# Performance work log

Hardware: AMD Instinct MI355X
Metric: run time of the kernel (lower is better)

Reference implementation:

```python
import jax, jax.numpy as jnp
import numpy as np
import math

HEAD_NUM = 16


def _split_qkv(qkv, head_num):
    # torch: rearrange(qkv, 'b t (d k h) -> k b h t d', k=3, h=head_num)
    B, T, E3 = qkv.shape
    d = E3 // (3 * head_num)
    qkv = qkv.reshape(B, T, d, 3, head_num)        # (b,t,d,k,h)
    qkv = jnp.transpose(qkv, (3, 0, 4, 1, 2))       # (k,b,h,t,d)
    return qkv[0], qkv[1], qkv[2]


def setup_inputs() -> dict:
    key = jax.random.key(0)
    ks = jax.random.split(key, 6)
    B, T, E = 4, 1024, 1024
    return {
        "x": jax.random.normal(ks[0], (B, T, E), dtype=jnp.float32),
        "y": jax.random.normal(ks[1], (B, T, E), dtype=jnp.float32),
        "Wqkv1": jax.random.normal(ks[2], (3 * E, E), dtype=jnp.float32) * 0.02,
        "Wqkv2": jax.random.normal(ks[3], (3 * E, E), dtype=jnp.float32) * 0.02,
        "Wout1": jax.random.normal(ks[4], (E, E), dtype=jnp.float32) * 0.02,
        "Wout2": jax.random.normal(ks[5], (E, E), dtype=jnp.float32) * 0.02,
    }


def reference(x, y, Wqkv1, Wqkv2, Wout1, Wout2):
    B, T, E = x.shape
    H = HEAD_NUM
    dk = math.sqrt(E / H)

    qkv1 = x @ Wqkv1.T                              # (B,T,3E)
    qkv2 = y @ Wqkv2.T
    q1, k1, v1 = _split_qkv(qkv1, H)                # each (B,H,T,d)
    q2, k2, v2 = _split_qkv(qkv2, H)

    # cross attention: stream-2 queries attend to stream-1 keys/values and vice versa
    energy1 = jnp.einsum('bhid,bhjd->bhij', q2, k1) / dk
    energy2 = jnp.einsum('bhid,bhjd->bhij', q1, k2) / dk
    attn1 = jax.nn.softmax(energy1, axis=-1)
    attn2 = jax.nn.softmax(energy2, axis=-1)

    xo = jnp.einsum('bhij,bhjd->bhid', attn1, v1)   # (B,H,T,d)
    yo = jnp.einsum('bhij,bhjd->bhid', attn2, v2)
    xo = jnp.transpose(xo, (0, 2, 1, 3)).reshape(B, T, E)  # b t (h d)
    yo = jnp.transpose(yo, (0, 2, 1, 3)).reshape(B, T, E)

    return xo @ Wout1.T, yo @ Wout2.T
```

## Files before the change

kernel.cpp:

```cpp
#include <hip/hip_runtime.h>
#include <hip/hip_bf16.h>

typedef __hip_bfloat16 bf16;
typedef __attribute__((ext_vector_type(8))) short short8;
typedef __attribute__((ext_vector_type(4))) short short4v;
typedef __attribute__((ext_vector_type(4))) float f32x4;

#define MFMA_BF16(a, b, c) __builtin_amdgcn_mfma_f32_16x16x32_bf16((a), (b), (c), 0, 0, 0)

#define QSCALE 0.1803368860111270f

__device__ __forceinline__ short f2bf(float f) {
    union { bf16 h; short s; } u;
    u.h = __float2bfloat16(f);
    return u.s;
}

#if defined(__has_builtin) && __has_builtin(__builtin_amdgcn_cvt_pk_bf16_f32)
typedef __attribute__((ext_vector_type(2))) __bf16 bf16x2_t;
__device__ __forceinline__ unsigned int pk2(float a, float b) {
    union { bf16x2_t v; unsigned int u; } x;
    x.v = __builtin_amdgcn_cvt_pk_bf16_f32(a, b);
    return x.u;
}
#else
__device__ __forceinline__ unsigned int pk2(float a, float b) {
    union { bf16 h[2]; unsigned int u; } x;
    x.h[0] = __float2bfloat16(a);
    x.h[1] = __float2bfloat16(b);
    return x.u;
}
#endif

#if defined(__has_builtin) && __has_builtin(__builtin_amdgcn_exp2f)
#define EXP2F(x) __builtin_amdgcn_exp2f(x)
#else
#define EXP2F(x) exp2f(x)
#endif

__device__ __forceinline__ void gload16(const void* g, void* l) {
    __builtin_amdgcn_global_load_lds(
        (const __attribute__((address_space(1))) unsigned int*)g,
        (__attribute__((address_space(3))) unsigned int*)l, 16, 0, 0);
}

__global__ void cvt_fused(const float* __restrict__ x, const float* __restrict__ y,
                          const float* __restrict__ wo1, const float* __restrict__ wo2,
                          const float* __restrict__ wq1, const float* __restrict__ wq2,
                          bf16* __restrict__ ox, bf16* __restrict__ oy,
                          bf16* __restrict__ oo1, bf16* __restrict__ oo2,
                          bf16* __restrict__ oq1, bf16* __restrict__ oq2) {
    const int yb = blockIdx.y;
    if (yb < 4) {
        int i = blockIdx.x * 256 + threadIdx.x;
        const float* src; bf16* dst; int n4;
        switch (yb) {
            case 0:  src = x;   dst = ox;  n4 = 1048576; break;
            case 1:  src = y;   dst = oy;  n4 = 1048576; break;
            case 2:  src = wo1; dst = oo1; n4 = 262144;  break;
            default: src = wo2; dst = oo2; n4 = 262144;  break;
        }
        if (i >= n4) return;
        float4 f = reinterpret_cast<const float4*>(src)[i];
        short4v s;
        s.x = f2bf(f.x); s.y = f2bf(f.y); s.z = f2bf(f.z); s.w = f2bf(f.w);
        reinterpret_cast<short4v*>(dst)[i] = s;
    } else {
        const int np = blockIdx.x;
        if (np >= 3072) return;
        const int comp = np >> 10, rem = np & 1023, h = rem >> 6, d = rem & 63;
        const int srow = d * 48 + comp * 16 + h;
        const float* src = ((yb == 5) ? wq2 : wq1) + (long)srow * 1024;
        bf16* dst = ((yb == 5) ? oq2 : oq1) + (long)np * 1024;
        const float sc = (comp == 0) ? QSCALE : 1.0f;
        int t = threadIdx.x;
        float4 f = reinterpret_cast<const float4*>(src)[t];
        short4v s;
        s.x = f2bf(f.x * sc); s.y = f2bf(f.y * sc); s.z = f2bf(f.z * sc); s.w = f2bf(f.w * sc);
        reinterpret_cast<short4v*>(dst)[t] = s;
    }
}

#define GATE4 do { asm volatile("s_waitcnt vmcnt(4)" ::: "memory"); \
    __builtin_amdgcn_s_barrier(); __builtin_amdgcn_sched_barrier(0); } while (0)

__global__ __launch_bounds__(512, 2)
void gemm_qkv256(const bf16* __restrict__ A0g, const bf16* __restrict__ B0g,
                 void* o0a, void* o0b, void* o0c,
                 const bf16* __restrict__ A1g, const bf16* __restrict__ B1g,
                 void* o1a, void* o1b, void* o1c) {
    extern __shared__ short smem[];
    const int z = blockIdx.z;
    const short* A = reinterpret_cast<const short*>(z ? A1g : A0g);
    const short* B = reinterpret_cast<const short*>(z ? B1g : B0g);
    const int tid  = threadIdx.x;
    const int lane = tid & 63;
    const int w    = tid >> 6;
    const int quad = lane >> 4;
    const int l16  = lane & 15;
    const long M0 = (long)blockIdx.y * 256;
    const long N0 = (long)blockIdx.x * 256;

    const int rowblk = (w >> 2) * 64;
    const int colblk = (w & 3) * 32;
    const int cA0  = (quad ^ (l16 & 7)) * 8;
    const int aoff = (rowblk + l16) * 64;
    const int boff = 16384 + (colblk + l16) * 64;
    const int w512 = w * 512;

    const short* Asrc = A + (M0 + w * 8 + (lane >> 3)) * 1024 + ((lane & 7) ^ (lane >> 3)) * 8;
    const short* Bsrc = B + (N0 + w * 8 + (lane >> 3)) * 1024 + ((lane & 7) ^ (lane >> 3)) * 8;

    f32x4 acc[4][4][2] = {};
    short8 af[4][2], bfv[2][2];

#define SA256(half, tt, nbase) do { \
    const short* _s = Asrc + (half) * 131072 + (tt) * 64; \
    short* _d = smem + (nbase) + (half) * 8192 + w512; \
    gload16(_s, _d); gload16(_s + 65536, _d + 4096); } while (0)
#define SB256(half, tt, nbase) do { \
    const short* _s = Bsrc + (half) * 131072 + (tt) * 64; \
    short* _d = smem + (nbase) + 16384 + (half) * 8192 + w512; \
    gload16(_s, _d); gload16(_s + 65536, _d + 4096); } while (0)
#define RDA256(Ah, bbv) do { \
    _Pragma("unroll") for (int mt = 0; mt < 4; ++mt) { \
        const short* _p = &smem[(bbv) + (Ah) * 8192 + aoff + mt * 1024]; \
        af[mt][0] = *reinterpret_cast<const short8*>(_p + cA0); \
        af[mt][1] = *reinterpret_cast<const short8*>(_p + (cA0 ^ 32)); } } while (0)
#define RDB256(Bh, bbv) do { \
    _Pragma("unroll") for (int nt = 0; nt < 2; ++nt) { \
        const short* _p = &smem[(bbv) + (Bh) * 8192 + boff + nt * 1024]; \
        bfv[nt][0] = *reinterpret_cast<const short8*>(_p + cA0); \
        bfv[nt][1] = *reinterpret_cast<const short8*>(_p + (cA0 ^ 32)); } } while (0)
#define MM256(p) do { \
    __builtin_amdgcn_s_setprio(1); \
    _Pragma("unroll") for (int mt = 0; mt < 4; ++mt) \
    _Pragma("unroll") for (int nt = 0; nt < 2; ++nt) { \
        acc[p][mt][nt] = MFMA_BF16(af[mt][0], bfv[nt][0], acc[p][mt][nt]); \
        acc[p][mt][nt] = MFMA_BF16(af[mt][1], bfv[nt][1], acc[p][mt][nt]); } \
    __builtin_amdgcn_s_setprio(0); } while (0)

    SA256(0, 0, 0); SB256(0, 0, 0); SB256(1, 0, 0); SA256(1, 0, 0);

#pragma unroll 1
    for (int t = 0; t < 15; ++t) {
        const int bb = (t & 1) << 15;
        const int nb = bb ^ 32768;
        GATE4;
        SA256(0, t + 1, nb);
        RDA256(0, bb); RDB256(0, bb);
        __builtin_amdgcn_sched_barrier(0);
        MM256(0);
        GATE4;
        SB256(0, t + 1, nb);
        RDB256(1, bb);
        __builtin_amdgcn_sched_barrier(0);
        MM256(1);
        GATE4;
        SB256(1, t + 1, nb);
        RDA256(1, bb); RDB256(0, bb);
        __builtin_amdgcn_sched_barrier(0);
        MM256(2);
        SA256(1, t + 1, nb);
        RDB256(1, bb);
        __builtin_amdgcn_sched_barrier(0);
        MM256(3);
    }
    asm volatile("s_waitcnt vmcnt(0)" ::: "memory");
    __builtin_amdgcn_s_barrier();
    __builtin_amdgcn_sched_barrier(0);
    {
        const int bb = 32768;
        RDA256(0, bb); RDB256(0, bb); MM256(0);
        RDB256(1, bb); MM256(1);
        RDA256(1, bb); RDB256(0, bb); MM256(2);
        RDB256(1, bb); MM256(3);
    }

    if (blockIdx.x < 8) {
        short* dst = reinterpret_cast<short*>(blockIdx.x < 4 ? (z ? o1a : o0a)
                                                             : (z ? o1b : o0b));
        const int b = (int)(M0 >> 10);
        const int t00 = ((int)M0 & 1023);
        const int hd00 = ((int)blockIdx.x & 3) * 256;
#pragma unroll
        for (int p = 0; p < 4; ++p) {
            const int Ah = p >> 1, Bh = p & 1;
            const int tr0 = t00 + Ah * 128 + rowblk + quad * 4;
#pragma unroll
            for (int nt = 0; nt < 2; ++nt) {
                const int hd = hd00 + Bh * 128 + colblk + nt * 16 + l16;
                const int h = hd >> 6, d = hd & 63;
                short* dp = dst + (long)(b * 16 + h) * 65536 + d;
#pragma unroll
                for (int mt = 0; mt < 4; ++mt)
#pragma unroll
                    for (int r = 0; r < 4; ++r)
                        dp[(long)(tr0 + mt * 16 + r) * 64] = f2bf(acc[p][mt][nt][r]);
            }
        }
    } else {
        short* vT = reinterpret_cast<short*>(z ? o1c : o0c);
        const int b = (int)(M0 >> 10);
        const int hd00 = ((int)blockIdx.x - 8) * 256;
        short* ws = smem + w * 2304;
        const int c8 = (lane & 7) * 8;
        const int colr = lane >> 3;
#pragma unroll
        for (int p = 0; p < 4; ++p) {
            const int Ah = p >> 1, Bh = p & 1;
#pragma unroll
            for (int nt = 0; nt < 2; ++nt)
#pragma unroll
                for (int mt = 0; mt < 4; ++mt) {
                    uint2 uu;
                    uu.x = pk2(acc[p][mt][nt][0], acc[p][mt][nt][1]);
                    uu.y = pk2(acc[p][mt][nt][2], acc[p][mt][nt][3]);
                    *reinterpret_cast<uint2*>(&ws[(nt * 16 + l16) * 72 + mt * 16 + quad * 4]) = uu;
                }
            const int tb = ((int)M0 & 1023) + Ah * 128 + rowblk + c8;
#pragma unroll
            for (int q4 = 0; q4 < 4; ++q4) {
                const int col = q4 * 8 + colr;
                const int hd = hd00 + Bh * 128 + colblk + col;
                const int h = hd >> 6, d = hd & 63;
                short8 v = *reinterpret_cast<const short8*>(&ws[col * 72 + c8]);
                *reinterpret_cast<short8*>(&vT[(long)(b * 16 + h) * 65536 + (long)d * 1024 + tb]) = v;
            }
        }
    }
#undef SA256
#undef SB256
#undef RDA256
#undef RDB256
#undef MM256
}

__global__ __launch_bounds__(256)
void gemm_out(const bf16* __restrict__ A0g, const bf16* __restrict__ B0g, float* __restrict__ C0,
              const bf16* __restrict__ A1g, const bf16* __restrict__ B1g, float* __restrict__ C1) {
    __shared__ short smem2[24576];
    const int z = blockIdx.z;
    const short* A = reinterpret_cast<const short*>(z ? A1g : A0g);
    const short* B = reinterpret_cast<const short*>(z ? B1g : B0g);
    const int tid  = threadIdx.x;
    const int lane = tid & 63;
    const int w    = tid >> 6;
    const int wr   = w >> 1;
    const int wc   = w & 1;
    const int quad = lane >> 4;
    const int l16  = lane & 15;
    const long bM = (long)blockIdx.y * 128;

    f32x4 acc[4][4] = {};

    const int sr  = lane >> 2;
    const int scs = ((lane & 3) ^ (sr & 3)) * 8;
    const short* Ag0 = A + (bM + 32 * w + sr) * 1024 + scs;
    const short* Ag1 = Ag0 + 16 * 1024;
    const short* Bg0 = B + ((long)blockIdx.x * 128 + 32 * w + sr) * 1024 + scs;
    const short* Bg1 = Bg0 + 16 * 1024;
    const int sq = (quad ^ (l16 & 3)) * 8;

    {
        short* sb = smem2;
        gload16(Ag0, sb + w * 1024);
        gload16(Ag1, sb + w * 1024 + 512);
        gload16(Bg0, sb + 4096 + w * 1024);
        gload16(Bg1, sb + 4096 + w * 1024 + 512);
    }

    int bcur = 0;
#pragma unroll 1
    for (int iter = 0; iter < 32; ++iter) {
        int bnext = bcur + 1; if (bnext == 3) bnext = 0;
        if (iter < 31) {
            const int koff = (iter + 1) * 32;
            short* sb = smem2 + bnext * 8192;
            gload16(Ag0 + koff, sb + w * 1024);
            gload16(Ag1 + koff, sb + w * 1024 + 512);
            gload16(Bg0 + koff, sb + 4096 + w * 1024);
            gload16(Bg1 + koff, sb + 4096 + w * 1024 + 512);
            asm volatile("s_waitcnt vmcnt(4)" ::: "memory");
        } else {
            asm volatile("s_waitcnt vmcnt(0)" ::: "memory");
        }
        __builtin_amdgcn_s_barrier();
        __builtin_amdgcn_sched_barrier(0);

        const short* Ab = smem2 + bcur * 8192;
        const short* Bb = Ab + 4096;

        short8 af[4], bfr[4];
#pragma unroll
        for (int mt = 0; mt < 4; ++mt)
            af[mt] = *reinterpret_cast<const short8*>(&Ab[(wr * 64 + mt * 16 + l16) * 32 + sq]);
#pragma unroll
        for (int nt = 0; nt < 4; ++nt)
            bfr[nt] = *reinterpret_cast<const short8*>(&Bb[(wc * 64 + nt * 16 + l16) * 32 + sq]);
        __builtin_amdgcn_s_setprio(1);
#pragma unroll
        for (int mt = 0; mt < 4; ++mt)
#pragma unroll
            for (int nt = 0; nt < 4; ++nt)
                acc[mt][nt] = MFMA_BF16(af[mt], bfr[nt], acc[mt][nt]);
        __builtin_amdgcn_s_setprio(0);
        bcur = bnext;
    }

    float* C = z ? C1 : C0;
    const long crow = bM + wr * 64 + quad * 4;
    const long ccol = (long)blockIdx.x * 128 + wc * 64 + l16;
#pragma unroll
    for (int mt = 0; mt < 4; ++mt)
#pragma unroll
        for (int nt = 0; nt < 4; ++nt)
#pragma unroll
            for (int r = 0; r < 4; ++r)
                C[(crow + mt * 16 + r) * 1024L + ccol + nt * 16] = acc[mt][nt][r];
}

__global__ __launch_bounds__(256)
void attn_kernel(const bf16* __restrict__ q0g, const bf16* __restrict__ k0g,
                 const bf16* __restrict__ v0g, bf16* __restrict__ o0g,
                 const bf16* __restrict__ q1g, const bf16* __restrict__ k1g,
                 const bf16* __restrict__ v1g, bf16* __restrict__ o1g) {
    __shared__ short smem[24576];
    const int bh = blockIdx.x;
    const int qt = blockIdx.y;
    const int z = blockIdx.z;
    const int b = bh >> 4, h = bh & 15;
    const int tid = threadIdx.x, lane = tid & 63, w = tid >> 6;
    const int quad = lane >> 4, l16 = lane & 15;

    const short* Qb = reinterpret_cast<const short*>(z ? q1g : q0g) + (long)bh * 1024 * 64;
    const short* Kb = reinterpret_cast<const short*>(z ? k1g : k0g) + (long)bh * 1024 * 64;
    const short* Vb = reinterpret_cast<const short*>(z ? v1g : v0g) + (long)bh * 64 * 1024;
    short* Ob = reinterpret_cast<short*>(z ? o1g : o0g);

    short8 qb[2][2];
#pragma unroll
    for (int qg = 0; qg < 2; ++qg) {
        const short* Qp = Qb + (long)(qt * 128 + qg * 64 + w * 16 + l16) * 64;
        qb[qg][0] = *reinterpret_cast<const short8*>(Qp + quad * 8);
        qb[qg][1] = *reinterpret_cast<const short8*>(Qp + 32 + quad * 8);
    }

    const int r8  = lane >> 3;
    const int sc0 = ((lane & 7) ^ (r8 & 3)) * 8;
    const short* Kg0 = Kb + (long)(16 * w + r8) * 64 + sc0;
    const short* Kg1 = Kb + (long)(16 * w + 8 + r8) * 64 + (sc0 ^ 32);
    const short* Vg0 = Vb + (long)(16 * w + r8) * 1024 + sc0;
    const short* Vg1 = Vb + (long)(16 * w + 8 + r8) * 1024 + (sc0 ^ 32);

    const int jbase = 8 * (l16 >> 2) + (l16 & 3);
    const int fKs = (l16 & 3) | (((l16 >> 2) & 1) << 2);
    const int s0  = (quad ^ fKs) * 8;
    const int fVs = (l16 & 3) | (((l16 >> 3) & 1) << 2);
    const int sv  = (quad ^ fVs) * 8;

    f32x4 o[2][4] = {};
    float li[2] = {0.f, 0.f};

    gload16(Kg0, smem + w * 1024); gload16(Kg1, smem + w * 1024 + 512);
    gload16(Vg0, smem + 4096 + w * 1024); gload16(Vg1, smem + 4096 + w * 1024 + 512);

    int bcur = 0;
#pragma unroll 1
    for (int iter = 0; iter < 16; ++iter) {
        int bnext = bcur + 1; if (bnext == 3) bnext = 0;
        if (iter < 15) {
            short* sb = smem + bnext * 8192;
            const long ko = (long)(iter + 1) * 4096;
            const long vo = (long)(iter + 1) * 64;
            gload16(Kg0 + ko, sb + w * 1024);
            gload16(Kg1 + ko, sb + w * 1024 + 512);
            gload16(Vg0 + vo, sb + 4096 + w * 1024);
            gload16(Vg1 + vo, sb + 4096 + w * 1024 + 512);
            asm volatile("s_waitcnt vmcnt(4)" ::: "memory");
        } else {
            asm volatile("s_waitcnt vmcnt(0)" ::: "memory");
        }
        __builtin_amdgcn_s_barrier();
        __builtin_amdgcn_sched_barrier(0);

        const short* Ks = smem + bcur * 8192;
        const short* Vs = Ks + 4096;

        f32x4 st[2][4];
        __builtin_amdgcn_s_setprio(1);
#pragma unroll
        for (int g = 0; g < 4; ++g) {
            const int goff = (g >> 1) * 32 + (g & 1) * 4;
            const short* kr = Ks + (jbase + goff) * 64;
            short8 k0 = *reinterpret_cast<const short8*>(kr + s0);
            short8 k1 = *reinterpret_cast<const short8*>(kr + (s0 ^ 32));
#pragma unroll
            for (int qg = 0; qg < 2; ++qg) {
                f32x4 zf = {0.f, 0.f, 0.f, 0.f};
                zf = MFMA_BF16(k0, qb[qg][0], zf);
                zf = MFMA_BF16(k1, qb[qg][1], zf);
                st[qg][g] = zf;
            }
        }
        __builtin_amdgcn_s_setprio(0);

        union { unsigned int u[4]; short8 s; } f0[2], f1[2];
#pragma unroll
        for (int qg = 0; qg < 2; ++qg) {
            float p[4][4];
            float rs = 0.f;
#pragma unroll
            for (int g = 0; g < 4; ++g)
#pragma unroll
                for (int r = 0; r < 4; ++r) {
                    float e = EXP2F(st[qg][g][r]);
                    p[g][r] = e;
                    rs += e;
                }
            li[qg] += rs;
            f0[qg].u[0] = pk2(p[0][0], p[0][1]); f0[qg].u[1] = pk2(p[0][2], p[0][3]);
            f0[qg].u[2] = pk2(p[1][0], p[1][1]); f0[qg].u[3] = pk2(p[1][2], p[1][3]);
            f1[qg].u[0] = pk2(p[2][0], p[2][1]); f1[qg].u[1] = pk2(p[2][2], p[2][3]);
            f1[qg].u[2] = pk2(p[3][0], p[3][1]); f1[qg].u[3] = pk2(p[3][2], p[3][3]);
        }

        __builtin_amdgcn_s_setprio(1);
#pragma unroll
        for (int dt = 0; dt < 4; ++dt) {
            const short* vr = Vs + (dt * 16 + l16) * 64;
            short8 v0 = *reinterpret_cast<const short8*>(vr + sv);
            short8 v1 = *reinterpret_cast<const short8*>(vr + (sv ^ 32));
#pragma unroll
            for (int qg = 0; qg < 2; ++qg) {
                o[qg][dt] = MFMA_BF16(v0, f0[qg].s, o[qg][dt]);
                o[qg][dt] = MFMA_BF16(v1, f1[qg].s, o[qg][dt]);
            }
        }
        __builtin_amdgcn_s_setprio(0);
        bcur = bnext;
    }

    __syncthreads();

#pragma unroll
    for (int qg = 0; qg < 2; ++qg) {
        li[qg] += __shfl_xor(li[qg], 16);
        li[qg] += __shfl_xor(li[qg], 32);
    }

#pragma unroll
    for (int qg = 0; qg < 2; ++qg) {
        short* Os = smem + qg * 5120 + w * 1280;
        const float rl = 1.0f / li[qg];
#pragma unroll
        for (int dt = 0; dt < 4; ++dt) {
            uint2 uu;
            uu.x = pk2(o[qg][dt][0] * rl, o[qg][dt][1] * rl);
            uu.y = pk2(o[qg][dt][2] * rl, o[qg][dt][3] * rl);
            *reinterpret_cast<uint2*>(&Os[l16 * 80 + dt * 16 + quad * 4]) = uu;
        }
#pragma unroll
        for (int p = 0; p < 2; ++p) {
            int row = p * 8 + (lane >> 3);
            int ch = (lane & 7) * 8;
            short8 v = *reinterpret_cast<const short8*>(&Os[row * 80 + ch]);
            *reinterpret_cast<short8*>(&Ob[((long)(b * 1024) + qt * 128 + qg * 64 + w * 16 + row) * 1024 + h * 64 + ch]) = v;
        }
    }
}

extern "C" void kernel_launch(void* const* d_in, const int* in_sizes, int n_in,
                              void* d_out, int out_size, void* d_ws, size_t ws_size,
                              hipStream_t stream) {
    const float* x     = (const float*)d_in[0];
    const float* y     = (const float*)d_in[1];
    const float* Wqkv1 = (const float*)d_in[2];
    const float* Wqkv2 = (const float*)d_in[3];
    const float* Wout1 = (const float*)d_in[4];
    const float* Wout2 = (const float*)d_in[5];

    char* ws = (char*)d_ws;
    bf16* Wqkv1b = (bf16*)(ws + 0);
    bf16* Wqkv2b = (bf16*)(ws + 6291456);
    bf16* Wout1b = (bf16*)(ws + 12582912);
    bf16* Wout2b = (bf16*)(ws + 14680064);
    bf16* xb     = (bf16*)(ws + 16777216);
    bf16* yb     = (bf16*)(ws + 25165824);
    bf16* q1     = (bf16*)(ws + 33554432);
    bf16* k1     = (bf16*)(ws + 41943040);
    bf16* v1T    = (bf16*)(ws + 50331648);
    bf16* q2     = (bf16*)(ws + 58720256);
    bf16* k2     = (bf16*)(ws + 67108864);
    bf16* v2T    = (bf16*)(ws + 75497472);
    bf16* xo     = xb;
    bf16* yo     = yb;

    static bool s_attr = false;
    if (!s_attr) {
        (void)hipFuncSetAttribute(reinterpret_cast<const void*>(&gemm_qkv256),
                                  hipFuncAttributeMaxDynamicSharedMemorySize, 131072);
        s_attr = true;
    }

    cvt_fused<<<dim3(4096, 6), 256, 0, stream>>>(x, y, Wout1, Wout2, Wqkv1, Wqkv2,
                                                 xb, yb, Wout1b, Wout2b, Wqkv1b, Wqkv2b);

    gemm_qkv256<<<dim3(12, 16, 2), 512, 131072, stream>>>(xb, Wqkv1b, q1, k1, v1T,
                                                          yb, Wqkv2b, q2, k2, v2T);

    attn_kernel<<<dim3(64, 8, 2), 256, 0, stream>>>(q2, k1, v1T, xo,
                                                    q1, k2, v2T, yo);

    gemm_out<<<dim3(8, 32, 2), 256, 0, stream>>>(xo, Wout1b, (float*)d_out,
                                                 yo, Wout2b, ((float*)d_out) + 4194304);
}
```

Baseline: 241.9 us.

## Shrink QKV GEMM tile to 128x256 to double block count

Changes the QKV projection GEMM from 256x256 to 128x256 output tiles per 512-thread block. The grid grows from 384 to 768 blocks, and LDS use drops from 128 KB to 96 KB. The pipeline is rebuilt as two phases per k-step with new vmcnt gates and a guarded final iteration. The aim is better load balance and occupancy across CUs, at the cost of less operand reuse per block and more global traffic for B.

```diff
diff --git a/kernel.cpp b/kernel.cpp
--- a/kernel.cpp
+++ b/kernel.cpp
@@ -81,11 +81,8 @@
     }
 }
 
-#define GATE4 do { asm volatile("s_waitcnt vmcnt(4)" ::: "memory"); \
-    __builtin_amdgcn_s_barrier(); __builtin_amdgcn_sched_barrier(0); } while (0)
-
 __global__ __launch_bounds__(512, 2)
-void gemm_qkv256(const bf16* __restrict__ A0g, const bf16* __restrict__ B0g,
+void gemm_qkv128(const bf16* __restrict__ A0g, const bf16* __restrict__ B0g,
                  void* o0a, void* o0b, void* o0c,
                  const bf16* __restrict__ A1g, const bf16* __restrict__ B1g,
                  void* o1a, void* o1b, void* o1c) {
@@ -98,41 +95,41 @@
     const int w    = tid >> 6;
     const int quad = lane >> 4;
     const int l16  = lane & 15;
-    const long M0 = (long)blockIdx.y * 256;
+    const long M0 = (long)blockIdx.y * 128;
     const long N0 = (long)blockIdx.x * 256;
 
-    const int rowblk = (w >> 2) * 64;
-    const int colblk = (w & 3) * 32;
+    const int wm = w >> 2;
+    const int wn = w & 3;
     const int cA0  = (quad ^ (l16 & 7)) * 8;
-    const int aoff = (rowblk + l16) * 64;
-    const int boff = 16384 + (colblk + l16) * 64;
+    const int aoff = wm * 4096 + l16 * 64;
+    const int boff = 8192 + wn * 2048 + l16 * 64;
     const int w512 = w * 512;
 
     const short* Asrc = A + (M0 + w * 8 + (lane >> 3)) * 1024 + ((lane & 7) ^ (lane >> 3)) * 8;
     const short* Bsrc = B + (N0 + w * 8 + (lane >> 3)) * 1024 + ((lane & 7) ^ (lane >> 3)) * 8;
 
-    f32x4 acc[4][4][2] = {};
+    f32x4 acc[2][4][2] = {};
     short8 af[4][2], bfv[2][2];
 
-#define SA256(half, tt, nbase) do { \
-    const short* _s = Asrc + (half) * 131072 + (tt) * 64; \
-    short* _d = smem + (nbase) + (half) * 8192 + w512; \
+#define SA128(tt, nbase) do { \
+    const short* _s = Asrc + (tt) * 64; \
+    short* _d = smem + (nbase) + w512; \
     gload16(_s, _d); gload16(_s + 65536, _d + 4096); } while (0)
-#define SB256(half, tt, nbase) do { \
+#define SB128(half, tt, nbase) do { \
     const short* _s = Bsrc + (half) * 131072 + (tt) * 64; \
-    short* _d = smem + (nbase) + 16384 + (half) * 8192 + w512; \
+    short* _d = smem + (nbase) + 8192 + (half) * 8192 + w512; \
     gload16(_s, _d); gload16(_s + 65536, _d + 4096); } while (0)
-#define RDA256(Ah, bbv) do { \
+#define RDA128(bbv) do { \
     _Pragma("unroll") for (int mt = 0; mt < 4; ++mt) { \
-        const short* _p = &smem[(bbv) + (Ah) * 8192 + aoff + mt * 1024]; \
+        const short* _p = &smem[(bbv) + aoff + mt * 1024]; \
         af[mt][0] = *reinterpret_cast<const short8*>(_p + cA0); \
         af[mt][1] = *reinterpret_cast<const short8*>(_p + (cA0 ^ 32)); } } while (0)
-#define RDB256(Bh, bbv) do { \
+#define RDB128(Bh, bbv) do { \
     _Pragma("unroll") for (int nt = 0; nt < 2; ++nt) { \
         const short* _p = &smem[(bbv) + (Bh) * 8192 + boff + nt * 1024]; \
         bfv[nt][0] = *reinterpret_cast<const short8*>(_p + cA0); \
         bfv[nt][1] = *reinterpret_cast<const short8*>(_p + (cA0 ^ 32)); } } while (0)
-#define MM256(p) do { \
+#define MM128(p) do { \
     __builtin_amdgcn_s_setprio(1); \
     _Pragma("unroll") for (int mt = 0; mt < 4; ++mt) \
     _Pragma("unroll") for (int nt = 0; nt < 2; ++nt) { \
@@ -140,100 +137,82 @@
         acc[p][mt][nt] = MFMA_BF16(af[mt][1], bfv[nt][1], acc[p][mt][nt]); } \
     __builtin_amdgcn_s_setprio(0); } while (0)
 
-    SA256(0, 0, 0); SB256(0, 0, 0); SB256(1, 0, 0); SA256(1, 0, 0);
+    SA128(0, 0); SB128(0, 0, 0); SB128(1, 0, 0);
 
 #pragma unroll 1
-    for (int t = 0; t < 15; ++t) {
-        const int bb = (t & 1) << 15;
-        const int nb = bb ^ 32768;
-        GATE4;
-        SA256(0, t + 1, nb);
-        RDA256(0, bb); RDB256(0, bb);
-        __builtin_amdgcn_sched_barrier(0);
-        MM256(0);
-        GATE4;
-        SB256(0, t + 1, nb);
-        RDB256(1, bb);
-        __builtin_amdgcn_sched_barrier(0);
-        MM256(1);
-        GATE4;
-        SB256(1, t + 1, nb);
-        RDA256(1, bb); RDB256(0, bb);
-        __builtin_amdgcn_sched_barrier(0);
-        MM256(2);
-        SA256(1, t + 1, nb);
-        RDB256(1, bb);
-        __builtin_amdgcn_sched_barrier(0);
-        MM256(3);
-    }
-    asm volatile("s_waitcnt vmcnt(0)" ::: "memory");
-    __builtin_amdgcn_s_barrier();
-    __builtin_amdgcn_sched_barrier(0);
-    {
-        const int bb = 32768;
-        RDA256(0, bb); RDB256(0, bb); MM256(0);
-        RDB256(1, bb); MM256(1);
-        RDA256(1, bb); RDB256(0, bb); MM256(2);
-        RDB256(1, bb); MM256(3);
+    for (int t = 0; t < 16; ++t) {
+        const int bb = (t & 1) ? 24576 : 0;
+        const int nb = bb ^ 24576;
+        asm volatile("s_waitcnt vmcnt(2)" ::: "memory");
+        __builtin_amdgcn_s_barrier();
+        __builtin_amdgcn_sched_barrier(0);
+        if (t < 15) { SA128(t + 1, nb); SB128(0, t + 1, nb); }
+        RDA128(bb); RDB128(0, bb);
+        __builtin_amdgcn_sched_barrier(0);
+        MM128(0);
+        if (t < 15) { asm volatile("s_waitcnt vmcnt(4)" ::: "memory"); }
+        else        { asm volatile("s_waitcnt vmcnt(0)" ::: "memory"); }
+        __builtin_amdgcn_s_barrier();
+        __builtin_amdgcn_sched_barrier(0);
+        if (t < 15) SB128(1, t + 1, nb);
+        RDB128(1, bb);
+        __builtin_amdgcn_sched_barrier(0);
+        MM128(1);
     }
 
     if (blockIdx.x < 8) {
         short* dst = reinterpret_cast<short*>(blockIdx.x < 4 ? (z ? o1a : o0a)
                                                              : (z ? o1b : o0b));
         const int b = (int)(M0 >> 10);
-        const int t00 = ((int)M0 & 1023);
-        const int hd00 = ((int)blockIdx.x & 3) * 256;
-#pragma unroll
-        for (int p = 0; p < 4; ++p) {
-            const int Ah = p >> 1, Bh = p & 1;
-            const int tr0 = t00 + Ah * 128 + rowblk + quad * 4;
+        const int t00 = ((int)M0 & 1023) + wm * 64 + quad * 4;
+        const int hd00 = ((int)blockIdx.x & 3) * 256 + wn * 32;
+#pragma unroll
+        for (int Bh = 0; Bh < 2; ++Bh)
 #pragma unroll
             for (int nt = 0; nt < 2; ++nt) {
-                const int hd = hd00 + Bh * 128 + colblk + nt * 16 + l16;
+                const int hd = hd00 + Bh * 128 + nt * 16 + l16;
                 const int h = hd >> 6, d = hd & 63;
                 short* dp = dst + (long)(b * 16 + h) * 65536 + d;
 #pragma unroll
                 for (int mt = 0; mt < 4; ++mt)
 #pragma unroll
                     for (int r = 0; r < 4; ++r)
-                        dp[(long)(tr0 + mt * 16 + r) * 64] = f2bf(acc[p][mt][nt][r]);
+                        dp[(long)(t00 + mt * 16 + r) * 64] = f2bf(acc[Bh][mt][nt][r]);
             }
-        }
     } else {
         short* vT = reinterpret_cast<short*>(z ? o1c : o0c);
         const int b = (int)(M0 >> 10);
-        const int hd00 = ((int)blockIdx.x - 8) * 256;
+        const int hd00 = ((int)blockIdx.x - 8) * 256 + wn * 32;
         short* ws = smem + w * 2304;
         const int c8 = (lane & 7) * 8;
         const int colr = lane >> 3;
-#pragma unroll
-        for (int p = 0; p < 4; ++p) {
-            const int Ah = p >> 1, Bh = p & 1;
+        const int tb = ((int)M0 & 1023) + wm * 64 + c8;
+#pragma unroll
+        for (int Bh = 0; Bh < 2; ++Bh) {
 #pragma unroll
             for (int nt = 0; nt < 2; ++nt)
 #pragma unroll
                 for (int mt = 0; mt < 4; ++mt) {
                     uint2 uu;
-                    uu.x = pk2(acc[p][mt][nt][0], acc[p][mt][nt][1]);
-                    uu.y = pk2(acc[p][mt][nt][2], acc[p][mt][nt][3]);
+                    uu.x = pk2(acc[Bh][mt][nt][0], acc[Bh][mt][nt][1]);
+                    uu.y = pk2(acc[Bh][mt][nt][2], acc[Bh][mt][nt][3]);
                     *reinterpret_cast<uint2*>(&ws[(nt * 16 + l16) * 72 + mt * 16 + quad * 4]) = uu;
                 }
-            const int tb = ((int)M0 & 1023) + Ah * 128 + rowblk + c8;
 #pragma unroll
             for (int q4 = 0; q4 < 4; ++q4) {
                 const int col = q4 * 8 + colr;
-                const int hd = hd00 + Bh * 128 + colblk + col;
+                const int hd = hd00 + Bh * 128 + col;
                 const int h = hd >> 6, d = hd & 63;
                 short8 v = *reinterpret_cast<const short8*>(&ws[col * 72 + c8]);
                 *reinterpret_cast<short8*>(&vT[(long)(b * 16 + h) * 65536 + (long)d * 1024 + tb]) = v;
             }
         }
     }
-#undef SA256
-#undef SB256
-#undef RDA256
-#undef RDB256
-#undef MM256
+#undef SA128
+#undef SB128
+#undef RDA128
+#undef RDB128
+#undef MM128
 }
 
 __global__ __launch_bounds__(256)
@@ -498,16 +477,16 @@
 
     static bool s_attr = false;
     if (!s_attr) {
-        (void)hipFuncSetAttribute(reinterpret_cast<const void*>(&gemm_qkv256),
-                                  hipFuncAttributeMaxDynamicSharedMemorySize, 131072);
+        (void)hipFuncSetAttribute(reinterpret_cast<const void*>(&gemm_qkv128),
+                                  hipFuncAttributeMaxDynamicSharedMemorySize, 98304);
         s_attr = true;
     }
 
     cvt_fused<<<dim3(4096, 6), 256, 0, stream>>>(x, y, Wout1, Wout2, Wqkv1, Wqkv2,
                                                  xb, yb, Wout1b, Wout2b, Wqkv1b, Wqkv2b);
 
-    gemm_qkv256<<<dim3(12, 16, 2), 512, 131072, stream>>>(xb, Wqkv1b, q1, k1, v1T,
-                                                          yb, Wqkv2b, q2, k2, v2T);
+    gemm_qkv128<<<dim3(12, 32, 2), 512, 98304, stream>>>(xb, Wqkv1b, q1, k1, v1T,
+                                                         yb, Wqkv2b, q2, k2, v2T);
 
     attn_kernel<<<dim3(64, 8, 2), 256, 0, stream>>>(q2, k1, v1T, xo,
                                                     q1, k2, v2T, yo);
```

Result: no change. 244.7 us (+1.1%).
